# Kernel tuning notes

Hardware: AMD Instinct MI355X
Metric: run time of the kernel (lower is better)

Reference implementation:

```python
import jax, jax.numpy as jnp
import numpy as np

SIGMAS = [0.5, 1.0, 2.0, 4.0, 8.0]
DATA_RANGE = 1.0
C1 = (0.01 * DATA_RANGE) ** 2
C2 = (0.03 * DATA_RANGE) ** 2
ALPHA = 0.025
COMPENSATION = 200.0
PAD = int(2 * SIGMAS[-1])            # 16
FILTER_SIZE = int(4 * SIGMAS[-1] + 1)  # 33


def _gauss_2d(size: int, sigma: float) -> np.ndarray:
    coords = np.arange(size, dtype=np.float32) - size // 2
    g = np.exp(-coords ** 2 / (2.0 * sigma ** 2))
    g /= g.sum()
    return np.outer(g, g)


def _make_g_masks() -> jnp.ndarray:
    # (3 * n_sigmas, 1, F, F): three identical masks per sigma, as in the torch buffer
    masks = np.zeros((3 * len(SIGMAS), 1, FILTER_SIZE, FILTER_SIZE), dtype=np.float32)
    for idx, sigma in enumerate(SIGMAS):
        k = _gauss_2d(FILTER_SIZE, sigma)
        masks[3 * idx + 0, 0] = k
        masks[3 * idx + 1, 0] = k
        masks[3 * idx + 2, 0] = k
    return jnp.asarray(masks)


def _gconv(x: jnp.ndarray, w: jnp.ndarray, groups: int) -> jnp.ndarray:
    return jax.lax.conv_general_dilated(
        x, w, window_strides=(1, 1), padding=[(PAD, PAD), (PAD, PAD)],
        dimension_numbers=("NCHW", "OIHW", "NCHW"), feature_group_count=groups)


def setup_inputs() -> dict:
    key = jax.random.key(0)
    k1, k2 = jax.random.split(key)
    img1 = jax.random.uniform(k1, (8, 3, 512, 512), dtype=jnp.float32)
    img2 = jax.random.uniform(k2, (8, 3, 512, 512), dtype=jnp.float32)
    return {"img1": img1, "img2": img2}


def reference(img1, img2):
    g_masks = _make_g_masks()
    ch = img1.shape[1]

    mux = _gconv(img1, g_masks, ch)           # (B, 15, H, W)
    muy = _gconv(img2, g_masks, ch)
    mux2 = mux * mux
    muy2 = muy * muy
    muxy = mux * muy
    sigmax2 = _gconv(img1 * img1, g_masks, ch) - mux2
    sigmay2 = _gconv(img2 * img2, g_masks, ch) - muy2
    sigmaxy = _gconv(img1 * img2, g_masks, ch) - muxy

    lc = (2.0 * muxy + C1) / (mux2 + muy2 + C1)
    cs = (2.0 * sigmaxy + C2) / (sigmax2 + sigmay2 + C2)

    lM = lc[:, -1] * lc[:, -2] * lc[:, -3]    # (B, H, W)
    PIcs = jnp.prod(cs, axis=1)               # (B, H, W)
    loss_ms_ssim = 1.0 - lM * PIcs

    loss_l1 = jnp.abs(img1 - img2)
    gaussian_l1 = _gconv(loss_l1, g_masks[-ch:], ch).mean(axis=1)  # (B, H, W)

    loss = ALPHA * loss_ms_ssim + (1.0 - ALPHA) * gaussian_l1 / DATA_RANGE
    return (COMPENSATION * loss).mean()
```

## Files before the change

kernel.cpp:

```cpp
#include <hip/hip_runtime.h>
#include <math.h>

struct GW { float w[171]; };
constexpr int W05 = 0;
constexpr int W1  = 21;
constexpr int W2  = 46;
constexpr int W4  = 81;
constexpr int W8  = 122;

namespace {

constexpr float kC1 = 1e-4f;
constexpr float kC2 = 9e-4f;


template<int R, int WOFF>
__device__ __forceinline__ void hpass4(const GW& g, const float* __restrict__ sS,
                                       const float* __restrict__ sD,
                                       float4* __restrict__ hb, int t) {
  constexpr int NROWS = 32 + 2 * R;
  constexpr int NE = NROWS * 8;
  constexpr int QS = (16 - R) & ~3;
  constexpr int NG = ((19 + R - QS) >> 2) + 1;
  if (t >= NE) return;
  const int hrow = t >> 3;
  const int cg = t & 7;
  const int srow = hrow + (16 - R);
  const int rx = srow & 7;
  const int rowbase = srow << 6;
  const int g0 = cg + (QS >> 2);
  float a0[4] = {0.f, 0.f, 0.f, 0.f}, a1[4] = {0.f, 0.f, 0.f, 0.f};
  float a2[4] = {0.f, 0.f, 0.f, 0.f}, a3[4] = {0.f, 0.f, 0.f, 0.f};
#pragma unroll 2
  for (int j = 0; j < NG; ++j) {
    const int off = rowbase + (((g0 + j) ^ rx) << 2);
    const int wb = WOFF + 8 + QS - 16 + R + 4 * j;
    const float4 s4 = *reinterpret_cast<const float4*>(&sS[off]);
    const float4 d4 = *reinterpret_cast<const float4*>(&sD[off]);
    const float* sp = reinterpret_cast<const float*>(&s4);
    const float* dp = reinterpret_cast<const float*>(&d4);
#pragma unroll
    for (int u = 0; u < 4; ++u) {
      const float sv = sp[u], dv = dp[u];
      const float s2 = sv * sv, d2 = dv * dv;
#pragma unroll
      for (int o = 0; o < 4; ++o) {
        const float wk = g.w[wb + u - o];
        a0[o] += wk * sv; a1[o] += wk * dv;
        a2[o] += wk * s2; a3[o] += wk * d2;
      }
    }
  }
  const int rb = hrow << 5;
#pragma unroll
  for (int o = 0; o < 4; ++o) {
    const int c = (cg << 2) + o;
    hb[rb + (c ^ ((c >> 3) & 3))] = make_float4(a0[o], a1[o], a2[o], a3[o]);
  }
}

template<int R, int WOFF>
__device__ __forceinline__ void vpass4(const GW& g, const float4* __restrict__ hb,
                                       int vc, int vr0,
                                       float (&o0)[2], float (&o1)[2],
                                       float (&o2)[2], float (&o3)[2]) {
#pragma unroll
  for (int i = 0; i < 2; ++i) { o0[i] = o1[i] = o2[i] = o3[i] = 0.f; }
  const int fc = vc ^ ((vc >> 3) & 3);
  const float4* __restrict__ hbp = hb + (vr0 << 5) + fc;
#pragma unroll 4
  for (int jj = 0; jj < 2 * R + 2; ++jj) {
    const float4 v = hbp[jj << 5];
    const int wb = WOFF + 8 + jj;
#pragma unroll
    for (int i = 0; i < 2; ++i) {
      const float wk = g.w[wb - i];
      o0[i] += wk * v.x; o1[i] += wk * v.y;
      o2[i] += wk * v.z; o3[i] += wk * v.w;
    }
  }
}

template<int R, int WOFF, int MULT, bool DOLM>
__device__ __forceinline__ void sweep4(const GW& g,
    const float* sS, const float* sD, float4* hb, int t, int vc, int vr0,
    float (&PI)[2], float (&lM)[2]) {
  __syncthreads();
  hpass4<R, WOFF>(g, sS, sD, hb, t);
  __syncthreads();
  float os[2], od[2], os2[2], od2[2];
  vpass4<R, WOFF>(g, hb, vc, vr0, os, od, os2, od2);
#pragma unroll
  for (int i = 0; i < 2; ++i) {
    const float vs = os2[i] - os[i] * os[i];
    const float vd = od2[i] - od[i] * od[i];
    const float cs = (0.5f * (vs - vd) + kC2) / (0.5f * (vs + vd) + kC2);
    float p = cs;
    if constexpr (MULT > 1) p *= cs;
    if constexpr (MULT > 2) p *= cs;
    PI[i] *= p;
    if constexpr (DOLM) {
      const float sa = os[i] * os[i], sb = od[i] * od[i];
      const float lc = (0.5f * (sa - sb) + kC1) / (0.5f * (sa + sb) + kC1);
      lM[i] = lc * lc * lc;
    }
  }
}

template<int R, int WOFF>
__device__ __forceinline__ void hpassL1(const GW& g, const float* __restrict__ sD,
                                        float* __restrict__ hbl, int t) {
  constexpr int QS = (16 - R) & ~3;
  constexpr int NG = ((19 + R - QS) >> 2) + 1;
  const int hrow = t >> 3;
  const int cg = t & 7;
  const int rx = hrow & 7;
  const int rowbase = hrow << 6;
  const int g0 = cg + (QS >> 2);
  float a0[4] = {0.f, 0.f, 0.f, 0.f};
#pragma unroll 2
  for (int j = 0; j < NG; ++j) {
    const int off = rowbase + (((g0 + j) ^ rx) << 2);
    const int wb = WOFF + 8 + QS - 16 + R + 4 * j;
    const float4 d4 = *reinterpret_cast<const float4*>(&sD[off]);
    const float* dp = reinterpret_cast<const float*>(&d4);
#pragma unroll
    for (int u = 0; u < 4; ++u) {
      const float av = dp[u];
#pragma unroll
      for (int o = 0; o < 4; ++o) a0[o] += g.w[wb + u - o] * av;
    }
  }
  *reinterpret_cast<float4*>(&hbl[(hrow << 5) + (cg << 2)]) =
      make_float4(a0[0], a0[1], a0[2], a0[3]);
}

template<int R, int WOFF>
__device__ __forceinline__ void sweepL1_fused(const GW& g, float* sD, float* hbl,
                                              const float (&al1)[8], int t,
                                              int vc, int vr0, float (&l1s)[2]) {
#pragma unroll
  for (int e = 0; e < 2; ++e) {
    const int gidx = t + (e << 9);
    const int ly = gidx >> 4, lg = gidx & 15;
    const int off = (ly << 6) + ((lg ^ (ly & 7)) << 2);
    *reinterpret_cast<float4*>(&sD[off]) =
        make_float4(al1[4 * e], al1[4 * e + 1], al1[4 * e + 2], al1[4 * e + 3]);
  }
  __syncthreads();
  hpassL1<R, WOFF>(g, sD, hbl, t);
  __syncthreads();
  const float* __restrict__ hblp = hbl + (vr0 << 5) + vc;
#pragma unroll 4
  for (int jj = 0; jj < 2 * R + 2; ++jj) {
    const float vl = hblp[jj << 5];
    const int wb = WOFF + 8 + jj;
#pragma unroll
    for (int i = 0; i < 2; ++i) l1s[i] += g.w[wb - i] * vl;
  }
}

__device__ __forceinline__ void load_tile(const float* __restrict__ p1,
                                          const float* __restrict__ p2,
                                          float* __restrict__ sS, float* __restrict__ sD,
                                          float (&al1)[8], int t, int gx0, int gy0) {
#pragma unroll 1
  for (int e = 0; e < 2; ++e) {
    const int gidx = t + (e << 9);
    const int ly = gidx >> 4, lg = gidx & 15;
    const int gy = gy0 + ly;
    const int gx = gx0 + (lg << 2);
    float4 a = make_float4(0.f, 0.f, 0.f, 0.f);
    float4 b = make_float4(0.f, 0.f, 0.f, 0.f);
    if (gy >= 0 && gy < 512) {
      if (gx >= 0 && gx + 3 < 512) {
        a = *reinterpret_cast<const float4*>(&p1[(gy << 9) + gx]);
        b = *reinterpret_cast<const float4*>(&p2[(gy << 9) + gx]);
      } else {
        float* ap = reinterpret_cast<float*>(&a);
        float* bp = reinterpret_cast<float*>(&b);
#pragma unroll
        for (int u = 0; u < 4; ++u) {
          const int x = gx + u;
          if (x >= 0 && x < 512) { ap[u] = p1[(gy << 9) + x]; bp[u] = p2[(gy << 9) + x]; }
        }
      }
    }
    float4 s, d;
    s.x = a.x + b.x; s.y = a.y + b.y; s.z = a.z + b.z; s.w = a.w + b.w;
    d.x = a.x - b.x; d.y = a.y - b.y; d.z = a.z - b.z; d.w = a.w - b.w;
    al1[4 * e + 0] += fabsf(d.x); al1[4 * e + 1] += fabsf(d.y);
    al1[4 * e + 2] += fabsf(d.z); al1[4 * e + 3] += fabsf(d.w);
    const int off = (ly << 6) + ((lg ^ (ly & 7)) << 2);
    *reinterpret_cast<float4*>(&sS[off]) = s;
    *reinterpret_cast<float4*>(&sD[off]) = d;
  }
}

}

extern "C" __global__ __launch_bounds__(512) void msssim_main(
    const float* __restrict__ img1, const float* __restrict__ img2,
    float* __restrict__ partial, GW g) {
  __shared__ __align__(16) float sS[4096];
  __shared__ __align__(16) float sD[4096];
  __shared__ __align__(16) float4 hb[2048];
  __shared__ float red[8];
  float* hbl = reinterpret_cast<float*>(hb);

  const int t = threadIdx.x;

  const int bid = (int)blockIdx.x + ((int)blockIdx.y << 4) + ((int)blockIdx.z << 8);
  const int swz = ((bid & 7) << 8) + (bid >> 3);
  const int bx = swz & 15, by = (swz >> 4) & 15, b = swz >> 8;

  const int gx0 = bx * 32 - 16;
  const int gy0 = by * 32 - 16;
  const int vc = t & 31;
  const int vr0 = (t >> 5) << 1;

  float PI[2] = {1.f, 1.f};
  float lM[2] = {0.f, 0.f};
  float l1s[2] = {0.f, 0.f};
  float al1[8] = {0.f, 0.f, 0.f, 0.f, 0.f, 0.f, 0.f, 0.f};

  {
    const float* p1 = img1 + (((size_t)b * 3 + 0) << 18);
    const float* p2 = img2 + (((size_t)b * 3 + 0) << 18);
    load_tile(p1, p2, sS, sD, al1, t, gx0, gy0);
    sweep4<2, W05, 3, false>(g, sS, sD, hb, t, vc, vr0, PI, lM);
    sweep4<4, W1, 2, false>(g, sS, sD, hb, t, vc, vr0, PI, lM);
  }
  {
    const float* p1 = img1 + (((size_t)b * 3 + 1) << 18);
    const float* p2 = img2 + (((size_t)b * 3 + 1) << 18);
    load_tile(p1, p2, sS, sD, al1, t, gx0, gy0);
    sweep4<4, W1, 1, false>(g, sS, sD, hb, t, vc, vr0, PI, lM);
    sweep4<9, W2, 3, false>(g, sS, sD, hb, t, vc, vr0, PI, lM);
    sweep4<12, W4, 1, false>(g, sS, sD, hb, t, vc, vr0, PI, lM);
  }
  {
    const float* p1 = img1 + (((size_t)b * 3 + 2) << 18);
    const float* p2 = img2 + (((size_t)b * 3 + 2) << 18);
    load_tile(p1, p2, sS, sD, al1, t, gx0, gy0);
    sweep4<12, W4, 2, false>(g, sS, sD, hb, t, vc, vr0, PI, lM);
    sweep4<16, W8, 3, true>(g, sS, sD, hb, t, vc, vr0, PI, lM);
  }
  sweepL1_fused<16, W8>(g, sD, hbl, al1, t, vc, vr0, l1s);

  float s = 0.f;
#pragma unroll
  for (int i = 0; i < 2; ++i)
    s += 0.025f * (1.f - lM[i] * PI[i]) + 0.975f * (l1s[i] * (1.f / 3.f));

#pragma unroll
  for (int off = 32; off >= 1; off >>= 1) s += __shfl_down(s, off, 64);
  if ((t & 63) == 0) red[t >> 6] = s;
  __syncthreads();
  if (t == 0) {
    float tot = 0.f;
#pragma unroll
    for (int i = 0; i < 8; ++i) tot += red[i];
    partial[swz] = tot;
  }
}

extern "C" __global__ __launch_bounds__(256) void msssim_reduce(
    const float* __restrict__ partial, float* __restrict__ out, int n) {
  __shared__ float red[4];
  float s = 0.f;
  for (int i = threadIdx.x; i < n; i += 256) s += partial[i];
#pragma unroll
  for (int off = 32; off >= 1; off >>= 1) s += __shfl_down(s, off, 64);
  if ((threadIdx.x & 63) == 0) red[threadIdx.x >> 6] = s;
  __syncthreads();
  if (threadIdx.x == 0) {
    out[0] = (red[0] + red[1] + red[2] + red[3]) * (200.0f / 2097152.0f);
  }
}

extern "C" void kernel_launch(void* const* d_in, const int* in_sizes, int n_in,
                              void* d_out, int out_size, void* d_ws, size_t ws_size,
                              hipStream_t stream) {
  const float* img1 = (const float*)d_in[0];
  const float* img2 = (const float*)d_in[1];
  float* out = (float*)d_out;
  float* partial = (float*)d_ws;

  GW g;
  {
    const double sig[5] = {0.5, 1.0, 2.0, 4.0, 8.0};
    const int R[5] = {2, 4, 9, 12, 16};
    const int off[5] = {W05, W1, W2, W4, W8};
    for (int i = 0; i < 5; ++i) {
      double tmp[17];
      double sum = 0.0;
      for (int k = 0; k <= R[i]; ++k) {
        tmp[k] = exp(-(double)(k * k) / (2.0 * sig[i] * sig[i]));
        sum += (k ? 2.0 : 1.0) * tmp[k];
      }
      const int len = 2 * R[i] + 17;
      for (int m = 0; m < len; ++m) {
        int d = m - 8 - R[i];
        if (d < 0) d = -d;
        g.w[off[i] + m] = (m >= 8 && m <= 8 + 2 * R[i]) ? (float)(tmp[d] / sum) : 0.0f;
      }
    }
  }

  dim3 grid(16, 16, 8);
  msssim_main<<<grid, dim3(512), 0, stream>>>(img1, img2, partial, g);
  msssim_reduce<<<1, dim3(256), 0, stream>>>(partial, out, 2048);
}
```

Measured before the change: 129.9 us.

## Store shared-memory tile and horizontal partials as packed fp16 to halve LDS footprint

Input sum/difference tiles and horizontal-pass intermediates are kept in shared memory as packed half2 instead of fp32. Arithmetic stays in fp32. This halves LDS usage (from about 64KB to 32KB) and LDS traffic, and the launch bounds now ask for more resident blocks per CU to raise occupancy. The cost is fp16 rounding of intermediates, which hurts the precision of the variance terms (E[x^2]-mu^2 cancellation). It also adds conversion instructions and extra barriers.

```diff
diff --git a/kernel.cpp b/kernel.cpp
--- a/kernel.cpp
+++ b/kernel.cpp
@@ -1,4 +1,5 @@
 #include <hip/hip_runtime.h>
+#include <hip/hip_fp16.h>
 #include <math.h>
 
 struct GW { float w[171]; };
@@ -14,10 +15,16 @@
 constexpr float kC2 = 9e-4f;
 
 
+__device__ __forceinline__ unsigned int h2u(__half2 h) {
+  union { __half2 h; unsigned int u; } cv; cv.h = h; return cv.u;
+}
+__device__ __forceinline__ __half2 u2h(unsigned int u) {
+  union { __half2 h; unsigned int u; } cv; cv.u = u; return cv.h;
+}
+
 template<int R, int WOFF>
-__device__ __forceinline__ void hpass4(const GW& g, const float* __restrict__ sS,
-                                       const float* __restrict__ sD,
-                                       float4* __restrict__ hb, int t) {
+__device__ __forceinline__ void hpass4(const GW& g, const __half2* __restrict__ sT,
+                                       uint2* __restrict__ hb, int t) {
   constexpr int NROWS = 32 + 2 * R;
   constexpr int NE = NROWS * 8;
   constexpr int QS = (16 - R) & ~3;
@@ -35,13 +42,12 @@
   for (int j = 0; j < NG; ++j) {
     const int off = rowbase + (((g0 + j) ^ rx) << 2);
     const int wb = WOFF + 8 + QS - 16 + R + 4 * j;
-    const float4 s4 = *reinterpret_cast<const float4*>(&sS[off]);
-    const float4 d4 = *reinterpret_cast<const float4*>(&sD[off]);
-    const float* sp = reinterpret_cast<const float*>(&s4);
-    const float* dp = reinterpret_cast<const float*>(&d4);
+    const float4 raw = *reinterpret_cast<const float4*>(&sT[off]);
+    const __half2* hp = reinterpret_cast<const __half2*>(&raw);
 #pragma unroll
     for (int u = 0; u < 4; ++u) {
-      const float sv = sp[u], dv = dp[u];
+      const float2 sd = __half22float2(hp[u]);
+      const float sv = sd.x, dv = sd.y;
       const float s2 = sv * sv, d2 = dv * dv;
 #pragma unroll
       for (int o = 0; o < 4; ++o) {
@@ -52,41 +58,44 @@
     }
   }
   const int rb = hrow << 5;
+  const int hx = hrow & 7;
 #pragma unroll
   for (int o = 0; o < 4; ++o) {
     const int c = (cg << 2) + o;
-    hb[rb + (c ^ ((c >> 3) & 3))] = make_float4(a0[o], a1[o], a2[o], a3[o]);
+    hb[rb + (c ^ hx)] = make_uint2(h2u(__floats2half2_rn(a0[o], a1[o])),
+                                   h2u(__floats2half2_rn(a2[o], a3[o])));
   }
 }
 
 template<int R, int WOFF>
-__device__ __forceinline__ void vpass4(const GW& g, const float4* __restrict__ hb,
+__device__ __forceinline__ void vpass4(const GW& g, const uint2* __restrict__ hb,
                                        int vc, int vr0,
                                        float (&o0)[2], float (&o1)[2],
                                        float (&o2)[2], float (&o3)[2]) {
 #pragma unroll
   for (int i = 0; i < 2; ++i) { o0[i] = o1[i] = o2[i] = o3[i] = 0.f; }
-  const int fc = vc ^ ((vc >> 3) & 3);
-  const float4* __restrict__ hbp = hb + (vr0 << 5) + fc;
 #pragma unroll 4
   for (int jj = 0; jj < 2 * R + 2; ++jj) {
-    const float4 v = hbp[jj << 5];
+    const int r = vr0 + jj;
+    const uint2 pk = hb[(r << 5) + (vc ^ (r & 7))];
+    const float2 sd = __half22float2(u2h(pk.x));
+    const float2 q  = __half22float2(u2h(pk.y));
     const int wb = WOFF + 8 + jj;
 #pragma unroll
     for (int i = 0; i < 2; ++i) {
       const float wk = g.w[wb - i];
-      o0[i] += wk * v.x; o1[i] += wk * v.y;
-      o2[i] += wk * v.z; o3[i] += wk * v.w;
+      o0[i] += wk * sd.x; o1[i] += wk * sd.y;
+      o2[i] += wk * q.x;  o3[i] += wk * q.y;
     }
   }
 }
 
 template<int R, int WOFF, int MULT, bool DOLM>
 __device__ __forceinline__ void sweep4(const GW& g,
-    const float* sS, const float* sD, float4* hb, int t, int vc, int vr0,
+    const __half2* sT, uint2* hb, int t, int vc, int vr0,
     float (&PI)[2], float (&lM)[2]) {
   __syncthreads();
-  hpass4<R, WOFF>(g, sS, sD, hb, t);
+  hpass4<R, WOFF>(g, sT, hb, t);
   __syncthreads();
   float os[2], od[2], os2[2], od2[2];
   vpass4<R, WOFF>(g, hb, vc, vr0, os, od, os2, od2);
@@ -108,52 +117,54 @@
 }
 
 template<int R, int WOFF>
-__device__ __forceinline__ void hpassL1(const GW& g, const float* __restrict__ sD,
-                                        float* __restrict__ hbl, int t) {
-  constexpr int QS = (16 - R) & ~3;
-  constexpr int NG = ((19 + R - QS) >> 2) + 1;
-  const int hrow = t >> 3;
-  const int cg = t & 7;
-  const int rx = hrow & 7;
-  const int rowbase = hrow << 6;
-  const int g0 = cg + (QS >> 2);
-  float a0[4] = {0.f, 0.f, 0.f, 0.f};
-#pragma unroll 2
-  for (int j = 0; j < NG; ++j) {
-    const int off = rowbase + (((g0 + j) ^ rx) << 2);
-    const int wb = WOFF + 8 + QS - 16 + R + 4 * j;
-    const float4 d4 = *reinterpret_cast<const float4*>(&sD[off]);
-    const float* dp = reinterpret_cast<const float*>(&d4);
-#pragma unroll
-    for (int u = 0; u < 4; ++u) {
-      const float av = dp[u];
-#pragma unroll
-      for (int o = 0; o < 4; ++o) a0[o] += g.w[wb + u - o] * av;
-    }
-  }
-  *reinterpret_cast<float4*>(&hbl[(hrow << 5) + (cg << 2)]) =
-      make_float4(a0[0], a0[1], a0[2], a0[3]);
-}
-
-template<int R, int WOFF>
-__device__ __forceinline__ void sweepL1_fused(const GW& g, float* sD, float* hbl,
+__device__ __forceinline__ void sweepL1_fused(const GW& g, uint2* hbmem,
                                               const float (&al1)[8], int t,
                                               int vc, int vr0, float (&l1s)[2]) {
+  __half* Lin = reinterpret_cast<__half*>(hbmem);
+  __half* Lout = reinterpret_cast<__half*>(hbmem) + 4096;
+  __syncthreads();
 #pragma unroll
   for (int e = 0; e < 2; ++e) {
     const int gidx = t + (e << 9);
     const int ly = gidx >> 4, lg = gidx & 15;
     const int off = (ly << 6) + ((lg ^ (ly & 7)) << 2);
-    *reinterpret_cast<float4*>(&sD[off]) =
-        make_float4(al1[4 * e], al1[4 * e + 1], al1[4 * e + 2], al1[4 * e + 3]);
-  }
-  __syncthreads();
-  hpassL1<R, WOFF>(g, sD, hbl, t);
-  __syncthreads();
-  const float* __restrict__ hblp = hbl + (vr0 << 5) + vc;
+    *reinterpret_cast<uint2*>(&Lin[off]) =
+        make_uint2(h2u(__floats2half2_rn(al1[4 * e], al1[4 * e + 1])),
+                   h2u(__floats2half2_rn(al1[4 * e + 2], al1[4 * e + 3])));
+  }
+  __syncthreads();
+  {
+    constexpr int QS = 0;
+    constexpr int NG = ((19 + R) >> 2) + 1;
+    const int hrow = t >> 3;
+    const int cg = t & 7;
+    const int rx = hrow & 7;
+    const int rowbase = hrow << 6;
+    const int g0 = cg;
+    float a0[4] = {0.f, 0.f, 0.f, 0.f};
+#pragma unroll 2
+    for (int j = 0; j < NG; ++j) {
+      const int off = rowbase + (((g0 + j) ^ rx) << 2);
+      const int wb = WOFF + 8 + QS - 16 + R + 4 * j;
+      const uint2 raw = *reinterpret_cast<const uint2*>(&Lin[off]);
+      const float2 v01 = __half22float2(u2h(raw.x));
+      const float2 v23 = __half22float2(u2h(raw.y));
+      const float vv[4] = {v01.x, v01.y, v23.x, v23.y};
+#pragma unroll
+      for (int u = 0; u < 4; ++u) {
+        const float av = vv[u];
+#pragma unroll
+        for (int o = 0; o < 4; ++o) a0[o] += g.w[wb + u - o] * av;
+      }
+    }
+    *reinterpret_cast<uint2*>(&Lout[(hrow << 5) + (cg << 2)]) =
+        make_uint2(h2u(__floats2half2_rn(a0[0], a0[1])),
+                   h2u(__floats2half2_rn(a0[2], a0[3])));
+  }
+  __syncthreads();
 #pragma unroll 4
   for (int jj = 0; jj < 2 * R + 2; ++jj) {
-    const float vl = hblp[jj << 5];
+    const float vl = __half2float(Lout[((vr0 + jj) << 5) + vc]);
     const int wb = WOFF + 8 + jj;
 #pragma unroll
     for (int i = 0; i < 2; ++i) l1s[i] += g.w[wb - i] * vl;
@@ -162,7 +173,7 @@
 
 __device__ __forceinline__ void load_tile(const float* __restrict__ p1,
                                           const float* __restrict__ p2,
-                                          float* __restrict__ sS, float* __restrict__ sD,
+                                          __half2* __restrict__ sT,
                                           float (&al1)[8], int t, int gx0, int gy0) {
 #pragma unroll 1
   for (int e = 0; e < 2; ++e) {
@@ -186,27 +197,26 @@
         }
       }
     }
-    float4 s, d;
-    s.x = a.x + b.x; s.y = a.y + b.y; s.z = a.z + b.z; s.w = a.w + b.w;
-    d.x = a.x - b.x; d.y = a.y - b.y; d.z = a.z - b.z; d.w = a.w - b.w;
-    al1[4 * e + 0] += fabsf(d.x); al1[4 * e + 1] += fabsf(d.y);
-    al1[4 * e + 2] += fabsf(d.z); al1[4 * e + 3] += fabsf(d.w);
+    const float sv[4] = {a.x + b.x, a.y + b.y, a.z + b.z, a.w + b.w};
+    const float dv[4] = {a.x - b.x, a.y - b.y, a.z - b.z, a.w - b.w};
+    al1[4 * e + 0] += fabsf(dv[0]); al1[4 * e + 1] += fabsf(dv[1]);
+    al1[4 * e + 2] += fabsf(dv[2]); al1[4 * e + 3] += fabsf(dv[3]);
+    __half2 tmp[4];
+#pragma unroll
+    for (int u = 0; u < 4; ++u) tmp[u] = __floats2half2_rn(sv[u], dv[u]);
     const int off = (ly << 6) + ((lg ^ (ly & 7)) << 2);
-    *reinterpret_cast<float4*>(&sS[off]) = s;
-    *reinterpret_cast<float4*>(&sD[off]) = d;
-  }
-}
-
-}
-
-extern "C" __global__ __launch_bounds__(512) void msssim_main(
+    *reinterpret_cast<float4*>(&sT[off]) = *reinterpret_cast<float4*>(tmp);
+  }
+}
+
+}
+
+extern "C" __global__ __launch_bounds__(512, 8) void msssim_main(
     const float* __restrict__ img1, const float* __restrict__ img2,
     float* __restrict__ partial, GW g) {
-  __shared__ __align__(16) float sS[4096];
-  __shared__ __align__(16) float sD[4096];
-  __shared__ __align__(16) float4 hb[2048];
+  __shared__ __align__(16) __half2 sT[4096];
+  __shared__ __align__(16) uint2 hb[2048];
   __shared__ float red[8];
-  float* hbl = reinterpret_cast<float*>(hb);
 
   const int t = threadIdx.x;
 
@@ -227,26 +237,28 @@
   {
     const float* p1 = img1 + (((size_t)b * 3 + 0) << 18);
     const float* p2 = img2 + (((size_t)b * 3 + 0) << 18);
-    load_tile(p1, p2, sS, sD, al1, t, gx0, gy0);
-    sweep4<2, W05, 3, false>(g, sS, sD, hb, t, vc, vr0, PI, lM);
-    sweep4<4, W1, 2, false>(g, sS, sD, hb, t, vc, vr0, PI, lM);
+    load_tile(p1, p2, sT, al1, t, gx0, gy0);
+    sweep4<2, W05, 3, false>(g, sT, hb, t, vc, vr0, PI, lM);
+    sweep4<4, W1, 2, false>(g, sT, hb, t, vc, vr0, PI, lM);
   }
   {
     const float* p1 = img1 + (((size_t)b * 3 + 1) << 18);
     const float* p2 = img2 + (((size_t)b * 3 + 1) << 18);
-    load_tile(p1, p2, sS, sD, al1, t, gx0, gy0);
-    sweep4<4, W1, 1, false>(g, sS, sD, hb, t, vc, vr0, PI, lM);
-    sweep4<9, W2, 3, false>(g, sS, sD, hb, t, vc, vr0, PI, lM);
-    sweep4<12, W4, 1, false>(g, sS, sD, hb, t, vc, vr0, PI, lM);
+    __syncthreads();
+    load_tile(p1, p2, sT, al1, t, gx0, gy0);
+    sweep4<4, W1, 1, false>(g, sT, hb, t, vc, vr0, PI, lM);
+    sweep4<9, W2, 3, false>(g, sT, hb, t, vc, vr0, PI, lM);
+    sweep4<12, W4, 1, false>(g, sT, hb, t, vc, vr0, PI, lM);
   }
   {
     const float* p1 = img1 + (((size_t)b * 3 + 2) << 18);
     const float* p2 = img2 + (((size_t)b * 3 + 2) << 18);
-    load_tile(p1, p2, sS, sD, al1, t, gx0, gy0);
-    sweep4<12, W4, 2, false>(g, sS, sD, hb, t, vc, vr0, PI, lM);
-    sweep4<16, W8, 3, true>(g, sS, sD, hb, t, vc, vr0, PI, lM);
-  }
-  sweepL1_fused<16, W8>(g, sD, hbl, al1, t, vc, vr0, l1s);
+    __syncthreads();
+    load_tile(p1, p2, sT, al1, t, gx0, gy0);
+    sweep4<12, W4, 2, false>(g, sT, hb, t, vc, vr0, PI, lM);
+    sweep4<16, W8, 3, true>(g, sT, hb, t, vc, vr0, PI, lM);
+  }
+  sweepL1_fused<16, W8>(g, hb, al1, t, vc, vr0, l1s);
 
   float s = 0.f;
 #pragma unroll
```

Result: slower. 154.8 us (+19.1%).

## Read image tiles directly from global memory in horizontal pass, drop LDS staging

Applied to the files above, without the earlier changes.

Removes the shared-memory staging of sum/difference tiles. Each horizontal pass now loads rows straight from global memory (relying on L1/L2 caching), computes s=a+b and d=a-b on the fly, and the L1 pass rereads all three channels. Edge blocks take a guarded-load variant while interior blocks use unguarded float4 loads. The launch bound asks for higher occupancy now that 32KB of LDS is gone, at the cost of repeated global/cache traffic and recomputed sums.

```diff
diff --git a/kernel.cpp b/kernel.cpp
--- a/kernel.cpp
+++ b/kernel.cpp
@@ -14,10 +14,23 @@
 constexpr float kC2 = 9e-4f;
 
 
-template<int R, int WOFF>
-__device__ __forceinline__ void hpass4(const GW& g, const float* __restrict__ sS,
-                                       const float* __restrict__ sD,
-                                       float4* __restrict__ hb, int t) {
+__device__ __forceinline__ float4 ld4_guard(const float* __restrict__ row, int cx) {
+  if (cx >= 0 && cx + 3 < 512) return *reinterpret_cast<const float4*>(row + cx);
+  float4 v = make_float4(0.f, 0.f, 0.f, 0.f);
+  float* vp = reinterpret_cast<float*>(&v);
+#pragma unroll
+  for (int u = 0; u < 4; ++u) {
+    const int x = cx + u;
+    if (x >= 0 && x < 512) vp[u] = row[x];
+  }
+  return v;
+}
+
+template<int R, int WOFF, bool EX>
+__device__ __forceinline__ void hpass_g(const GW& g, const float* __restrict__ p1,
+                                        const float* __restrict__ p2,
+                                        float4* __restrict__ hb, int t,
+                                        int gx0, int gy0) {
   constexpr int NROWS = 32 + 2 * R;
   constexpr int NE = NROWS * 8;
   constexpr int QS = (16 - R) & ~3;
@@ -25,29 +38,34 @@
   if (t >= NE) return;
   const int hrow = t >> 3;
   const int cg = t & 7;
-  const int srow = hrow + (16 - R);
-  const int rx = srow & 7;
-  const int rowbase = srow << 6;
-  const int g0 = cg + (QS >> 2);
+  const int gy = gy0 + hrow + (16 - R);
   float a0[4] = {0.f, 0.f, 0.f, 0.f}, a1[4] = {0.f, 0.f, 0.f, 0.f};
   float a2[4] = {0.f, 0.f, 0.f, 0.f}, a3[4] = {0.f, 0.f, 0.f, 0.f};
+  if (gy >= 0 && gy < 512) {
+    const float* __restrict__ r1 = p1 + ((size_t)gy << 9);
+    const float* __restrict__ r2 = p2 + ((size_t)gy << 9);
+    const int c0 = gx0 + ((cg + (QS >> 2)) << 2);
 #pragma unroll 2
-  for (int j = 0; j < NG; ++j) {
-    const int off = rowbase + (((g0 + j) ^ rx) << 2);
-    const int wb = WOFF + 8 + QS - 16 + R + 4 * j;
-    const float4 s4 = *reinterpret_cast<const float4*>(&sS[off]);
-    const float4 d4 = *reinterpret_cast<const float4*>(&sD[off]);
-    const float* sp = reinterpret_cast<const float*>(&s4);
-    const float* dp = reinterpret_cast<const float*>(&d4);
-#pragma unroll
-    for (int u = 0; u < 4; ++u) {
-      const float sv = sp[u], dv = dp[u];
-      const float s2 = sv * sv, d2 = dv * dv;
-#pragma unroll
-      for (int o = 0; o < 4; ++o) {
-        const float wk = g.w[wb + u - o];
-        a0[o] += wk * sv; a1[o] += wk * dv;
-        a2[o] += wk * s2; a3[o] += wk * d2;
+    for (int j = 0; j < NG; ++j) {
+      const int cx = c0 + (j << 2);
+      float4 a, bb;
+      if constexpr (EX) { a = ld4_guard(r1, cx); bb = ld4_guard(r2, cx); }
+      else { a = *reinterpret_cast<const float4*>(r1 + cx);
+             bb = *reinterpret_cast<const float4*>(r2 + cx); }
+      const int wb = WOFF + 8 + QS - 16 + R + 4 * j;
+      const float* ap = reinterpret_cast<const float*>(&a);
+      const float* bp = reinterpret_cast<const float*>(&bb);
+#pragma unroll
+      for (int u = 0; u < 4; ++u) {
+        const float sv = ap[u] + bp[u];
+        const float dv = ap[u] - bp[u];
+        const float s2 = sv * sv, d2 = dv * dv;
+#pragma unroll
+        for (int o = 0; o < 4; ++o) {
+          const float wk = g.w[wb + u - o];
+          a0[o] += wk * sv; a1[o] += wk * dv;
+          a2[o] += wk * s2; a3[o] += wk * d2;
+        }
       }
     }
   }
@@ -81,12 +99,13 @@
   }
 }
 
-template<int R, int WOFF, int MULT, bool DOLM>
-__device__ __forceinline__ void sweep4(const GW& g,
-    const float* sS, const float* sD, float4* hb, int t, int vc, int vr0,
-    float (&PI)[2], float (&lM)[2]) {
-  __syncthreads();
-  hpass4<R, WOFF>(g, sS, sD, hb, t);
+template<int R, int WOFF, int MULT, bool DOLM, bool EX>
+__device__ __forceinline__ void sweep4(const GW& g, const float* p1, const float* p2,
+                                       float4* hb, int t, int vc, int vr0,
+                                       int gx0, int gy0,
+                                       float (&PI)[2], float (&lM)[2]) {
+  __syncthreads();
+  hpass_g<R, WOFF, EX>(g, p1, p2, hb, t, gx0, gy0);
   __syncthreads();
   float os[2], od[2], os2[2], od2[2];
   vpass4<R, WOFF>(g, hb, vc, vr0, os, od, os2, od2);
@@ -107,48 +126,52 @@
   }
 }
 
-template<int R, int WOFF>
-__device__ __forceinline__ void hpassL1(const GW& g, const float* __restrict__ sD,
-                                        float* __restrict__ hbl, int t) {
-  constexpr int QS = (16 - R) & ~3;
-  constexpr int NG = ((19 + R - QS) >> 2) + 1;
-  const int hrow = t >> 3;
-  const int cg = t & 7;
-  const int rx = hrow & 7;
-  const int rowbase = hrow << 6;
-  const int g0 = cg + (QS >> 2);
-  float a0[4] = {0.f, 0.f, 0.f, 0.f};
+template<int R, int WOFF, bool EX>
+__device__ __forceinline__ void sweepL1_g(const GW& g, const float* base1,
+                                          const float* base2, float* hbl, int t,
+                                          int vc, int vr0, int gx0, int gy0,
+                                          float (&l1s)[2]) {
+  constexpr int QS = 0;
+  constexpr int NG = ((19 + R) >> 2) + 1;
+  __syncthreads();
+  {
+    const int hrow = t >> 3;
+    const int cg = t & 7;
+    const int gy = gy0 + hrow;
+    float a0[4] = {0.f, 0.f, 0.f, 0.f};
+    if (gy >= 0 && gy < 512) {
+      const size_t rowoff = (size_t)gy << 9;
+      const int c0 = gx0 + (cg << 2);
 #pragma unroll 2
-  for (int j = 0; j < NG; ++j) {
-    const int off = rowbase + (((g0 + j) ^ rx) << 2);
-    const int wb = WOFF + 8 + QS - 16 + R + 4 * j;
-    const float4 d4 = *reinterpret_cast<const float4*>(&sD[off]);
-    const float* dp = reinterpret_cast<const float*>(&d4);
-#pragma unroll
-    for (int u = 0; u < 4; ++u) {
-      const float av = dp[u];
-#pragma unroll
-      for (int o = 0; o < 4; ++o) a0[o] += g.w[wb + u - o] * av;
-    }
-  }
-  *reinterpret_cast<float4*>(&hbl[(hrow << 5) + (cg << 2)]) =
-      make_float4(a0[0], a0[1], a0[2], a0[3]);
-}
-
-template<int R, int WOFF>
-__device__ __forceinline__ void sweepL1_fused(const GW& g, float* sD, float* hbl,
-                                              const float (&al1)[8], int t,
-                                              int vc, int vr0, float (&l1s)[2]) {
-#pragma unroll
-  for (int e = 0; e < 2; ++e) {
-    const int gidx = t + (e << 9);
-    const int ly = gidx >> 4, lg = gidx & 15;
-    const int off = (ly << 6) + ((lg ^ (ly & 7)) << 2);
-    *reinterpret_cast<float4*>(&sD[off]) =
-        make_float4(al1[4 * e], al1[4 * e + 1], al1[4 * e + 2], al1[4 * e + 3]);
-  }
-  __syncthreads();
-  hpassL1<R, WOFF>(g, sD, hbl, t);
+      for (int j = 0; j < NG; ++j) {
+        const int cx = c0 + (j << 2);
+        float4 av[3], bv[3];
+#pragma unroll
+        for (int ch = 0; ch < 3; ++ch) {
+          const float* r1 = base1 + ((size_t)ch << 18) + rowoff;
+          const float* r2 = base2 + ((size_t)ch << 18) + rowoff;
+          if constexpr (EX) { av[ch] = ld4_guard(r1, cx); bv[ch] = ld4_guard(r2, cx); }
+          else { av[ch] = *reinterpret_cast<const float4*>(r1 + cx);
+                 bv[ch] = *reinterpret_cast<const float4*>(r2 + cx); }
+        }
+        const int wb = WOFF + 8 + QS - 16 + R + 4 * j;
+#pragma unroll
+        for (int u = 0; u < 4; ++u) {
+          float sum = 0.f;
+#pragma unroll
+          for (int ch = 0; ch < 3; ++ch) {
+            const float* ap = reinterpret_cast<const float*>(&av[ch]);
+            const float* bp = reinterpret_cast<const float*>(&bv[ch]);
+            sum += fabsf(ap[u] - bp[u]);
+          }
+#pragma unroll
+          for (int o = 0; o < 4; ++o) a0[o] += g.w[wb + u - o] * sum;
+        }
+      }
+    }
+    *reinterpret_cast<float4*>(&hbl[(hrow << 5) + (cg << 2)]) =
+        make_float4(a0[0], a0[1], a0[2], a0[3]);
+  }
   __syncthreads();
   const float* __restrict__ hblp = hbl + (vr0 << 5) + vc;
 #pragma unroll 4
@@ -160,53 +183,33 @@
   }
 }
 
-__device__ __forceinline__ void load_tile(const float* __restrict__ p1,
-                                          const float* __restrict__ p2,
-                                          float* __restrict__ sS, float* __restrict__ sD,
-                                          float (&al1)[8], int t, int gx0, int gy0) {
-#pragma unroll 1
-  for (int e = 0; e < 2; ++e) {
-    const int gidx = t + (e << 9);
-    const int ly = gidx >> 4, lg = gidx & 15;
-    const int gy = gy0 + ly;
-    const int gx = gx0 + (lg << 2);
-    float4 a = make_float4(0.f, 0.f, 0.f, 0.f);
-    float4 b = make_float4(0.f, 0.f, 0.f, 0.f);
-    if (gy >= 0 && gy < 512) {
-      if (gx >= 0 && gx + 3 < 512) {
-        a = *reinterpret_cast<const float4*>(&p1[(gy << 9) + gx]);
-        b = *reinterpret_cast<const float4*>(&p2[(gy << 9) + gx]);
-      } else {
-        float* ap = reinterpret_cast<float*>(&a);
-        float* bp = reinterpret_cast<float*>(&b);
-#pragma unroll
-        for (int u = 0; u < 4; ++u) {
-          const int x = gx + u;
-          if (x >= 0 && x < 512) { ap[u] = p1[(gy << 9) + x]; bp[u] = p2[(gy << 9) + x]; }
-        }
-      }
-    }
-    float4 s, d;
-    s.x = a.x + b.x; s.y = a.y + b.y; s.z = a.z + b.z; s.w = a.w + b.w;
-    d.x = a.x - b.x; d.y = a.y - b.y; d.z = a.z - b.z; d.w = a.w - b.w;
-    al1[4 * e + 0] += fabsf(d.x); al1[4 * e + 1] += fabsf(d.y);
-    al1[4 * e + 2] += fabsf(d.z); al1[4 * e + 3] += fabsf(d.w);
-    const int off = (ly << 6) + ((lg ^ (ly & 7)) << 2);
-    *reinterpret_cast<float4*>(&sS[off]) = s;
-    *reinterpret_cast<float4*>(&sD[off]) = d;
-  }
-}
-
-}
-
-extern "C" __global__ __launch_bounds__(512) void msssim_main(
+template<bool EX>
+__device__ __forceinline__ void run_all(const GW& g, const float* base1,
+                                        const float* base2, float4* hb, int t,
+                                        int vc, int vr0, int gx0, int gy0,
+                                        float (&PI)[2], float (&lM)[2],
+                                        float (&l1s)[2]) {
+  const float* c0a = base1;                const float* c0b = base2;
+  const float* c1a = base1 + (1 << 18);    const float* c1b = base2 + (1 << 18);
+  const float* c2a = base1 + (2 << 18);    const float* c2b = base2 + (2 << 18);
+  sweep4<2, W05, 3, false, EX>(g, c0a, c0b, hb, t, vc, vr0, gx0, gy0, PI, lM);
+  sweep4<4, W1, 2, false, EX>(g, c0a, c0b, hb, t, vc, vr0, gx0, gy0, PI, lM);
+  sweep4<4, W1, 1, false, EX>(g, c1a, c1b, hb, t, vc, vr0, gx0, gy0, PI, lM);
+  sweep4<9, W2, 3, false, EX>(g, c1a, c1b, hb, t, vc, vr0, gx0, gy0, PI, lM);
+  sweep4<12, W4, 1, false, EX>(g, c1a, c1b, hb, t, vc, vr0, gx0, gy0, PI, lM);
+  sweep4<12, W4, 2, false, EX>(g, c2a, c2b, hb, t, vc, vr0, gx0, gy0, PI, lM);
+  sweep4<16, W8, 3, true, EX>(g, c2a, c2b, hb, t, vc, vr0, gx0, gy0, PI, lM);
+  sweepL1_g<16, W8, EX>(g, base1, base2, reinterpret_cast<float*>(hb), t,
+                        vc, vr0, gx0, gy0, l1s);
+}
+
+}
+
+extern "C" __global__ __launch_bounds__(512, 8) void msssim_main(
     const float* __restrict__ img1, const float* __restrict__ img2,
     float* __restrict__ partial, GW g) {
-  __shared__ __align__(16) float sS[4096];
-  __shared__ __align__(16) float sD[4096];
   __shared__ __align__(16) float4 hb[2048];
   __shared__ float red[8];
-  float* hbl = reinterpret_cast<float*>(hb);
 
   const int t = threadIdx.x;
 
@@ -222,31 +225,15 @@
   float PI[2] = {1.f, 1.f};
   float lM[2] = {0.f, 0.f};
   float l1s[2] = {0.f, 0.f};
-  float al1[8] = {0.f, 0.f, 0.f, 0.f, 0.f, 0.f, 0.f, 0.f};
-
-  {
-    const float* p1 = img1 + (((size_t)b * 3 + 0) << 18);
-    const float* p2 = img2 + (((size_t)b * 3 + 0) << 18);
-    load_tile(p1, p2, sS, sD, al1, t, gx0, gy0);
-    sweep4<2, W05, 3, false>(g, sS, sD, hb, t, vc, vr0, PI, lM);
-    sweep4<4, W1, 2, false>(g, sS, sD, hb, t, vc, vr0, PI, lM);
-  }
-  {
-    const float* p1 = img1 + (((size_t)b * 3 + 1) << 18);
-    const float* p2 = img2 + (((size_t)b * 3 + 1) << 18);
-    load_tile(p1, p2, sS, sD, al1, t, gx0, gy0);
-    sweep4<4, W1, 1, false>(g, sS, sD, hb, t, vc, vr0, PI, lM);
-    sweep4<9, W2, 3, false>(g, sS, sD, hb, t, vc, vr0, PI, lM);
-    sweep4<12, W4, 1, false>(g, sS, sD, hb, t, vc, vr0, PI, lM);
-  }
-  {
-    const float* p1 = img1 + (((size_t)b * 3 + 2) << 18);
-    const float* p2 = img2 + (((size_t)b * 3 + 2) << 18);
-    load_tile(p1, p2, sS, sD, al1, t, gx0, gy0);
-    sweep4<12, W4, 2, false>(g, sS, sD, hb, t, vc, vr0, PI, lM);
-    sweep4<16, W8, 3, true>(g, sS, sD, hb, t, vc, vr0, PI, lM);
-  }
-  sweepL1_fused<16, W8>(g, sD, hbl, al1, t, vc, vr0, l1s);
+
+  const float* base1 = img1 + ((size_t)b * 3 << 18);
+  const float* base2 = img2 + ((size_t)b * 3 << 18);
+
+  if (bx == 0 || bx == 15) {
+    run_all<true>(g, base1, base2, hb, t, vc, vr0, gx0, gy0, PI, lM, l1s);
+  } else {
+    run_all<false>(g, base1, base2, hb, t, vc, vr0, gx0, gy0, PI, lM, l1s);
+  }
 
   float s = 0.f;
 #pragma unroll
```

Result: slower. 362.5 us (+179.0%).
